# Optimization experiments

Hardware: AMD Instinct MI355X
Metric: run time of the kernel (lower is better)

## Reference

```python
import jax, jax.numpy as jnp
import numpy as np

N, E, G = 30000, 120000, 256
F_IN, F_E, H, T = 16, 8, 32, 10
EPS = 1e-5


def setup_inputs() -> dict:
    key = jax.random.key(0)
    ks = jax.random.split(key, 16)
    s = 0.05
    inp = {
        'x': jax.random.normal(ks[0], (N, F_IN), jnp.float32),
        'edge_attr': jax.random.normal(ks[1], (E, F_E), jnp.float32),
        'edge_index': jax.random.randint(ks[2], (2, E), 0, N),
        'batch': jnp.sort(jax.random.randint(ks[3], (N,), 0, G)),
        'c1_nn_w': jax.random.normal(ks[4], (F_E, F_IN * H), jnp.float32) * s,
        'c1_nn_b': jnp.zeros((F_IN * H,), jnp.float32),
        'c1_root': jax.random.normal(ks[5], (F_IN, H), jnp.float32) * s,
        'c1_bias': jnp.zeros((H,), jnp.float32),
        'c2_nn_w': jax.random.normal(ks[6], (F_E, H * H), jnp.float32) * s,
        'c2_nn_b': jnp.zeros((H * H,), jnp.float32),
        'c2_root': jax.random.normal(ks[7], (H, H), jnp.float32) * s,
        'c2_bias': jnp.zeros((H,), jnp.float32),
        'c3_nn_w': jax.random.normal(ks[8], (F_E, H * H), jnp.float32) * s,
        'c3_nn_b': jnp.zeros((H * H,), jnp.float32),
        'c3_root': jax.random.normal(ks[9], (H, H), jnp.float32) * s,
        'c3_bias': jnp.zeros((H,), jnp.float32),
        'bn1_g': jnp.ones((H,), jnp.float32), 'bn1_b': jnp.zeros((H,), jnp.float32),
        'bn1_m': jnp.zeros((H,), jnp.float32), 'bn1_v': jnp.ones((H,), jnp.float32),
        'bn2_g': jnp.ones((H,), jnp.float32), 'bn2_b': jnp.zeros((H,), jnp.float32),
        'bn2_m': jnp.zeros((H,), jnp.float32), 'bn2_v': jnp.ones((H,), jnp.float32),
        'mlp_w1': jax.random.normal(ks[10], (H, H), jnp.float32) * s,
        'mlp_b1': jnp.zeros((H,), jnp.float32),
        'mlp_w2': jax.random.normal(ks[11], (H, T), jnp.float32) * s,
        'mlp_b2': jnp.zeros((T,), jnp.float32),
    }
    return inp


def _nnconv(x, edge_index, edge_attr, nn_w, nn_b, root, bias, in_dim, out_dim):
    # per-edge weight matrix from edge features: [E, in_dim, out_dim]
    W = (edge_attr @ nn_w + nn_b).reshape(-1, in_dim, out_dim)
    # gather source node features, per-edge matvec, scatter-add to targets
    msg = jnp.einsum('ei,eio->eo', x[edge_index[0]], W)
    agg = jax.ops.segment_sum(msg, edge_index[1], num_segments=N)
    return agg + x @ root + bias


def _graph_size_norm(x, batch):
    deg = jax.ops.segment_sum(jnp.ones((N,), x.dtype), batch, num_segments=G)
    inv_sqrt = jnp.where(deg > 0, deg, 1.0) ** -0.5
    return x * inv_sqrt[batch][:, None]


def _bn_eval(x, g, b, m, v):
    return (x - m) * (g * jax.lax.rsqrt(v + EPS)) + b


def reference(x, edge_attr, edge_index, batch,
              c1_nn_w, c1_nn_b, c1_root, c1_bias,
              c2_nn_w, c2_nn_b, c2_root, c2_bias,
              c3_nn_w, c3_nn_b, c3_root, c3_bias,
              bn1_g, bn1_b, bn1_m, bn1_v,
              bn2_g, bn2_b, bn2_m, bn2_v,
              mlp_w1, mlp_b1, mlp_w2, mlp_b2):
    h = _nnconv(x, edge_index, edge_attr, c1_nn_w, c1_nn_b, c1_root, c1_bias, F_IN, H)
    h = _graph_size_norm(h, batch)
    h = jax.nn.relu(_bn_eval(h, bn1_g, bn1_b, bn1_m, bn1_v))
    h = _nnconv(h, edge_index, edge_attr, c2_nn_w, c2_nn_b, c2_root, c2_bias, H, H)
    h = _graph_size_norm(h, batch)
    h = jax.nn.relu(_bn_eval(h, bn2_g, bn2_b, bn2_m, bn2_v))
    h = _nnconv(h, edge_index, edge_attr, c3_nn_w, c3_nn_b, c3_root, c3_bias, H, H)
    # global mean pool over graphs
    cnt = jax.ops.segment_sum(jnp.ones((N,), h.dtype), batch, num_segments=G)
    pooled = jax.ops.segment_sum(h, batch, num_segments=G) / jnp.maximum(cnt, 1.0)[:, None]
    # MLP head (dropout inactive in eval)
    out = jax.nn.relu(pooled @ mlp_w1 + mlp_b1) @ mlp_w2 + mlp_b2
    return out
```

## Files before the change

### kernel.cpp

```cpp
#include <hip/hip_runtime.h>

#define NN 30000
#define NE 120000
#define NG 256
#define FIN 16
#define HD 32
#define TOUT 10
#define EPSV 1e-5f
#define NB_SCAN 30

__device__ __forceinline__ void atomAddF(float* p, float v) {
    unsafeAtomicAdd(p, v);
}

__global__ __launch_bounds__(256) void count_deg_kernel(
    const int* __restrict__ eidx, const int* __restrict__ batch,
    int* __restrict__ deg_in, float* __restrict__ deg_g)
{
    const int t = blockIdx.x * 256 + threadIdx.x;
    if (t < NE) atomicAdd(&deg_in[eidx[NE + t]], 1);

    const int lane = threadIdx.x & 63;
    const int g = (t < NN) ? batch[t] : -1;
    const int prev = __shfl_up(g, 1);
    const bool head = (lane == 0) || (g != prev);
    const unsigned long long heads = __ballot(head);
    if (head && g >= 0) {
        const unsigned long long higher =
            (lane < 63) ? (heads >> (lane + 1)) : 0ULL;
        const int next = higher ? (lane + __ffsll(higher)) : 64;
        atomAddF(&deg_g[g], (float)(next - lane));
    }
}

__global__ __launch_bounds__(1024) void scan_phase1(
    const int* __restrict__ deg_in, int* __restrict__ row_start,
    int* __restrict__ blocksum)
{
    __shared__ int wsum[16];
    const int t = threadIdx.x, lane = t & 63, w = t >> 6;
    const int idx = blockIdx.x * 1024 + t;
    const int v = (idx < NN) ? deg_in[idx] : 0;
    int s = v;
    #pragma unroll
    for (int off = 1; off < 64; off <<= 1) {
        const int u = __shfl_up(s, off, 64);
        if (lane >= off) s += u;
    }
    if (lane == 63) wsum[w] = s;
    __syncthreads();
    if (w == 0) {
        int ws = (lane < 16) ? wsum[lane] : 0;
        #pragma unroll
        for (int off = 1; off < 16; off <<= 1) {
            const int u = __shfl_up(ws, off, 64);
            if (lane >= off) ws += u;
        }
        if (lane < 16) wsum[lane] = ws;
    }
    __syncthreads();
    const int incl = s + ((w > 0) ? wsum[w - 1] : 0);
    if (idx < NN) row_start[idx] = incl - v;
    if (t == 1023) blocksum[blockIdx.x] = incl;
}

__global__ __launch_bounds__(1024) void scan_apply(
    const int* __restrict__ blocksum, int* __restrict__ row_start,
    int* __restrict__ cursor)
{
    __shared__ int boff_s;
    const int t = threadIdx.x;
    if (t < 64) {
        int v = (t < blockIdx.x) ? blocksum[t] : 0;
        #pragma unroll
        for (int off = 32; off > 0; off >>= 1) v += __shfl_down(v, off, 64);
        if (t == 0) boff_s = v;
    }
    __syncthreads();
    const int idx = blockIdx.x * 1024 + t;
    if (idx < NN) {
        const int r = row_start[idx] + boff_s;
        row_start[idx] = r;
        cursor[idx]    = r;
    }
    if (blockIdx.x == 0 && t == 0) row_start[NN] = NE;
}

__global__ __launch_bounds__(256) void csr_scatter(
    const int* __restrict__ eidx, const float* __restrict__ ea,
    int* __restrict__ cursor,
    int* __restrict__ src_s,
    float4* __restrict__ ea_s)
{
    const int e = blockIdx.x * 256 + threadIdx.x;
    if (e < NE) {
        const int d = eidx[NE + e];
        const int slot = atomicAdd(&cursor[d], 1);
        src_s[slot] = eidx[e];
        const float4* s4 = (const float4*)(ea + (size_t)e * 8);
        ea_s[2 * slot]     = s4[0];
        ea_s[2 * slot + 1] = s4[1];
    }
    if (e < 8) src_s[NE + e] = 0;
}

template<int IN, bool FINAL>
__global__ __launch_bounds__(256, 8) void fused_layer(
    const float* __restrict__ hin,
    const int*   __restrict__ src_s,
    const float4* __restrict__ ea_s,
    const int*   __restrict__ row_start,
    const float* __restrict__ nn_w,
    const float* __restrict__ nn_b,
    const float* __restrict__ root,
    const float* __restrict__ bias,
    const int*   __restrict__ batch,
    const float* __restrict__ deg_g,
    const float* __restrict__ bn_g,
    const float* __restrict__ bn_b,
    const float* __restrict__ bn_m,
    const float* __restrict__ bn_v,
    float*       __restrict__ out)
{
    constexpr int K  = 10 * IN;
    constexpr int KQ = K / 4;
    constexpr int KL = KQ / 2;
    constexpr int NQ = 32 / IN;

    __shared__ float Tlds[16 * K];
    __shared__ float Acc[16 * 32];

    const int tid = threadIdx.x;
    const int wv  = tid >> 6;
    const int l   = tid & 63;
    const int h   = l >> 5;
    const int o   = l & 31;
    const int l5  = l & 31;
    const int pr  = l >> 5;

    Acc[tid]       = bias[tid & 31];
    Acc[256 + tid] = bias[tid & 31];

    const int i = l5 & (IN - 1);
    const int q = l5 / IN;

    #pragma unroll
    for (int j = 0; j < 2; ++j) {
        const int nloc = wv * 4 + j * 2 + pr;
        const int d    = blockIdx.x * 16 + nloc;

        float t[9];
        #pragma unroll
        for (int f = 0; f < 9; ++f) t[f] = 0.0f;

        const int p0 = row_start[d];
        const int p1 = row_start[d + 1];

        int p = p0 + q;
        if (p < p1) {
            int pn     = p + NQ;
            int s_cur  = src_s[p];
            int s_nxt  = src_s[pn];
            float4 a_c = ea_s[2 * p];
            float4 b_c = ea_s[2 * p + 1];
            float  xv  = hin[(long)s_cur * IN + i];

            while (true) {
                const float4 a_n = ea_s[2 * pn];
                const float4 b_n = ea_s[2 * pn + 1];
                const float  xvn = hin[(long)s_nxt * IN + i];
                const int pn2    = pn + NQ;
                const int s_n2   = src_s[pn2];

                t[0] = fmaf(a_c.x, xv, t[0]);
                t[1] = fmaf(a_c.y, xv, t[1]);
                t[2] = fmaf(a_c.z, xv, t[2]);
                t[3] = fmaf(a_c.w, xv, t[3]);
                t[4] = fmaf(b_c.x, xv, t[4]);
                t[5] = fmaf(b_c.y, xv, t[5]);
                t[6] = fmaf(b_c.z, xv, t[6]);
                t[7] = fmaf(b_c.w, xv, t[7]);
                t[8] += xv;

                p = pn;
                if (p >= p1) break;
                pn = pn2; s_nxt = s_n2;
                a_c = a_n; b_c = b_n; xv = xvn;
            }
        }

        if (IN == 16) {
            #pragma unroll
            for (int f = 0; f < 9; ++f) t[f] += __shfl_xor(t[f], 16, 64);
        }

        if (l5 < IN) {
            float* tb = Tlds + nloc * K;
            #pragma unroll
            for (int f = 0; f < 9; ++f) tb[f * IN + i] = t[f];
            tb[9 * IN + i] = hin[(long)d * IN + i];
        }
    }
    __syncthreads();

    float Wreg[KL];
    const int kbase = wv * KQ + h * KL;
    #pragma unroll
    for (int kk = 0; kk < KL; ++kk) {
        const int k = kbase + kk;
        const float* src = (k < 8 * IN) ? (nn_w + k * 32)
                         : (k < 9 * IN) ? (nn_b + (k - 8 * IN) * 32)
                                        : (root + (k - 9 * IN) * 32);
        Wreg[kk] = src[o];
    }

    for (int n = 0; n < 16; ++n) {
        const float* tb = Tlds + n * K + kbase;
        float acc = 0.0f;
        #pragma unroll
        for (int kq = 0; kq < KL / 4; ++kq) {
            const float4 tv = *(const float4*)(tb + kq * 4);
            acc = fmaf(Wreg[4 * kq + 0], tv.x, acc);
            acc = fmaf(Wreg[4 * kq + 1], tv.y, acc);
            acc = fmaf(Wreg[4 * kq + 2], tv.z, acc);
            acc = fmaf(Wreg[4 * kq + 3], tv.w, acc);
        }
        acc += __shfl_xor(acc, 32, 64);
        if (h == 0) atomicAdd(&Acc[n * 32 + o], acc);
    }
    __syncthreads();

    #pragma unroll
    for (int r = 0; r < 2; ++r) {
        const int idx = r * 256 + tid;
        const int n   = idx >> 5;
        const int oo  = idx & 31;
        float sum = Acc[idx];
        const int d = blockIdx.x * 16 + n;
        const int g = batch[d];
        if (!FINAL) {
            float dg = deg_g[g];
            dg = dg > 0.0f ? dg : 1.0f;
            float v = sum * (1.0f / sqrtf(dg));
            const float s = bn_g[oo] / sqrtf(bn_v[oo] + EPSV);
            v = (v - bn_m[oo]) * s + bn_b[oo];
            out[(long)d * 32 + oo] = v > 0.0f ? v : 0.0f;
        } else {
            float v = sum;
            const int   g2 = __shfl(g, (tid & 63) ^ 32, 64);
            const float v2 = __shfl(v, (tid & 63) ^ 32, 64);
            bool do_store = true;
            if (g2 == g) {
                if (tid & 32) do_store = false;
                else          v += v2;
            }
            if (do_store) atomAddF(&out[g * 32 + oo], v);
        }
    }
}

__global__ __launch_bounds__(64) void head_kernel(
    const float* __restrict__ pooled,
    const float* __restrict__ deg,
    const float* __restrict__ w1,
    const float* __restrict__ b1,
    const float* __restrict__ w2,
    const float* __restrict__ b2,
    float*       __restrict__ out)
{
    const int g = blockIdx.x * 64 + threadIdx.x;
    if (g >= NG) return;
    float cnt = deg[g];
    cnt = cnt > 1.0f ? cnt : 1.0f;

    float p[HD];
    #pragma unroll
    for (int i = 0; i < HD; ++i) p[i] = pooled[g * HD + i] / cnt;

    float hid[HD];
    #pragma unroll
    for (int j = 0; j < HD; ++j) {
        float a = b1[j];
        #pragma unroll
        for (int i = 0; i < HD; ++i)
            a = fmaf(p[i], w1[i * HD + j], a);
        hid[j] = a > 0.0f ? a : 0.0f;
    }
    #pragma unroll
    for (int t = 0; t < TOUT; ++t) {
        float a = b2[t];
        #pragma unroll
        for (int j = 0; j < HD; ++j)
            a = fmaf(hid[j], w2[j * TOUT + t], a);
        out[g * TOUT + t] = a;
    }
}

extern "C" void kernel_launch(void* const* d_in, const int* in_sizes, int n_in,
                              void* d_out, int out_size, void* d_ws, size_t ws_size,
                              hipStream_t stream)
{
    const float* x        = (const float*)d_in[0];
    const float* ea       = (const float*)d_in[1];
    const int*   eidx     = (const int*)  d_in[2];
    const int*   batch    = (const int*)  d_in[3];
    const float* c1_nn_w  = (const float*)d_in[4];
    const float* c1_nn_b  = (const float*)d_in[5];
    const float* c1_root  = (const float*)d_in[6];
    const float* c1_bias  = (const float*)d_in[7];
    const float* c2_nn_w  = (const float*)d_in[8];
    const float* c2_nn_b  = (const float*)d_in[9];
    const float* c2_root  = (const float*)d_in[10];
    const float* c2_bias  = (const float*)d_in[11];
    const float* c3_nn_w  = (const float*)d_in[12];
    const float* c3_nn_b  = (const float*)d_in[13];
    const float* c3_root  = (const float*)d_in[14];
    const float* c3_bias  = (const float*)d_in[15];
    const float* bn1_g    = (const float*)d_in[16];
    const float* bn1_b    = (const float*)d_in[17];
    const float* bn1_m    = (const float*)d_in[18];
    const float* bn1_v    = (const float*)d_in[19];
    const float* bn2_g    = (const float*)d_in[20];
    const float* bn2_b    = (const float*)d_in[21];
    const float* bn2_m    = (const float*)d_in[22];
    const float* bn2_v    = (const float*)d_in[23];
    const float* mlp_w1   = (const float*)d_in[24];
    const float* mlp_b1   = (const float*)d_in[25];
    const float* mlp_w2   = (const float*)d_in[26];
    const float* mlp_b2   = (const float*)d_in[27];
    float* out = (float*)d_out;

    float4* ea_s   = (float4*)d_ws;
    int*    src_s  = (int*)(ea_s + 2 * (NE + 8));
    float*  h1     = (float*)(src_s + NE + 8);
    float*  h2     = h1 + NN * HD;
    int*    deg_in = (int*)(h2 + NN * HD);
    float*  deg_g  = (float*)(deg_in + NN);
    float*  pooled = deg_g + NG;
    int*    row_s  = (int*)(pooled + NG * HD);
    int*    cursor = row_s + NN + 1;
    int*    bsum   = cursor + NN;

    hipMemsetAsync(deg_in, 0, sizeof(int) * (NN + NG + NG * HD), stream);

    const int egrid = (NE + 255) / 256;

    count_deg_kernel<<<egrid, 256, 0, stream>>>(eidx, batch, deg_in, deg_g);
    scan_phase1<<<NB_SCAN, 1024, 0, stream>>>(deg_in, row_s, bsum);
    scan_apply <<<NB_SCAN, 1024, 0, stream>>>(bsum, row_s, cursor);
    csr_scatter<<<egrid, 256, 0, stream>>>(eidx, ea, cursor, src_s, ea_s);

    const int lgrid = NN / 16;

    fused_layer<FIN, false><<<lgrid, 256, 0, stream>>>(
        x, src_s, ea_s, row_s, c1_nn_w, c1_nn_b, c1_root, c1_bias,
        batch, deg_g, bn1_g, bn1_b, bn1_m, bn1_v, h1);

    fused_layer<HD, false><<<lgrid, 256, 0, stream>>>(
        h1, src_s, ea_s, row_s, c2_nn_w, c2_nn_b, c2_root, c2_bias,
        batch, deg_g, bn2_g, bn2_b, bn2_m, bn2_v, h2);

    fused_layer<HD, true><<<lgrid, 256, 0, stream>>>(
        h2, src_s, ea_s, row_s, c3_nn_w, c3_nn_b, c3_root, c3_bias,
        batch, deg_g, nullptr, nullptr, nullptr, nullptr, pooled);

    head_kernel<<<(NG + 63) / 64, 64, 0, stream>>>(pooled, deg_g, mlp_w1, mlp_b1,
                                                   mlp_w2, mlp_b2, out);
}
```

Measured before the change: 274.6 us.

## Distribute block's edges flat across threads with LDS atomic accumulation

Instead of assigning a fixed group of lanes to each destination node, each block now walks the contiguous range of all edges belonging to its 16 nodes, with threads striding by 256/IN edges. Partial products go straight into padded shared-memory rows through LDS atomics, and the CSR now stores (src,dst) pairs so each edge knows its target row. The aim is to remove load imbalance and idle lanes on nodes with few or many edges. The cost is nine shared atomics per edge per feature, possible contention when edges hit the same row, and a larger edge array.

```diff
diff --git a/kernel.cpp b/kernel.cpp
--- a/kernel.cpp
+++ b/kernel.cpp
@@ -89,25 +89,30 @@
 __global__ __launch_bounds__(256) void csr_scatter(
     const int* __restrict__ eidx, const float* __restrict__ ea,
     int* __restrict__ cursor,
-    int* __restrict__ src_s,
+    int2* __restrict__ sd_s,
     float4* __restrict__ ea_s)
 {
     const int e = blockIdx.x * 256 + threadIdx.x;
     if (e < NE) {
+        const int s = eidx[e];
         const int d = eidx[NE + e];
         const int slot = atomicAdd(&cursor[d], 1);
-        src_s[slot] = eidx[e];
+        sd_s[slot] = make_int2(s, d);
         const float4* s4 = (const float4*)(ea + (size_t)e * 8);
         ea_s[2 * slot]     = s4[0];
         ea_s[2 * slot + 1] = s4[1];
     }
-    if (e < 8) src_s[NE + e] = 0;
+    if (e < 32) {
+        sd_s[NE + e] = make_int2(0, 0);
+        ea_s[2 * (NE + e)]     = make_float4(0.f, 0.f, 0.f, 0.f);
+        ea_s[2 * (NE + e) + 1] = make_float4(0.f, 0.f, 0.f, 0.f);
+    }
 }
 
 template<int IN, bool FINAL>
 __global__ __launch_bounds__(256, 8) void fused_layer(
     const float* __restrict__ hin,
-    const int*   __restrict__ src_s,
+    const int2*  __restrict__ sd_s,
     const float4* __restrict__ ea_s,
     const int*   __restrict__ row_start,
     const float* __restrict__ nn_w,
@@ -122,83 +127,77 @@
     const float* __restrict__ bn_v,
     float*       __restrict__ out)
 {
-    constexpr int K  = 10 * IN;
-    constexpr int KQ = K / 4;
-    constexpr int KL = KQ / 2;
-    constexpr int NQ = 32 / IN;
-
-    __shared__ float Tlds[16 * K];
+    constexpr int K   = 10 * IN;
+    constexpr int KP  = K + 4;
+    constexpr int KQ  = K / 4;
+    constexpr int KL  = K / 8;
+    constexpr int EPG = 256 / IN;
+
+    __shared__ float Tlds[16 * KP];
     __shared__ float Acc[16 * 32];
 
-    const int tid = threadIdx.x;
-    const int wv  = tid >> 6;
-    const int l   = tid & 63;
-    const int h   = l >> 5;
-    const int o   = l & 31;
-    const int l5  = l & 31;
-    const int pr  = l >> 5;
-
-    Acc[tid]       = bias[tid & 31];
-    Acc[256 + tid] = bias[tid & 31];
-
-    const int i = l5 & (IN - 1);
-    const int q = l5 / IN;
-
-    #pragma unroll
-    for (int j = 0; j < 2; ++j) {
-        const int nloc = wv * 4 + j * 2 + pr;
-        const int d    = blockIdx.x * 16 + nloc;
-
-        float t[9];
-        #pragma unroll
-        for (int f = 0; f < 9; ++f) t[f] = 0.0f;
-
-        const int p0 = row_start[d];
-        const int p1 = row_start[d + 1];
-
-        int p = p0 + q;
-        if (p < p1) {
-            int pn     = p + NQ;
-            int s_cur  = src_s[p];
-            int s_nxt  = src_s[pn];
-            float4 a_c = ea_s[2 * p];
-            float4 b_c = ea_s[2 * p + 1];
-            float  xv  = hin[(long)s_cur * IN + i];
+    const int tid  = threadIdx.x;
+    const int wv   = tid >> 6;
+    const int l    = tid & 63;
+    const int h    = l >> 5;
+    const int o    = l & 31;
+    const int base = blockIdx.x * 16;
+
+    {
+        float4* tz = (float4*)Tlds;
+        constexpr int NZ4 = (16 * 9 * IN) / 4;
+        constexpr int C4  = (9 * IN) / 4;
+        for (int idx = tid; idx < NZ4; idx += 256) {
+            const int n = idx / C4;
+            const int c = idx % C4;
+            tz[n * (KP / 4) + c] = make_float4(0.f, 0.f, 0.f, 0.f);
+        }
+        #pragma unroll
+        for (int r = 0; r < (16 * IN) / 256; ++r) {
+            const int idx = r * 256 + tid;
+            Tlds[(idx / IN) * KP + 9 * IN + (idx % IN)] =
+                hin[(long)base * IN + idx];
+        }
+        Acc[tid]       = bias[o];
+        Acc[256 + tid] = bias[o];
+    }
+    __syncthreads();
+
+    {
+        const int i = tid % IN;
+        const int s = tid / IN;
+        const int e0 = row_start[base];
+        const int e1 = row_start[base + 16];
+
+        int p = e0 + s;
+        if (p < e1) {
+            int2   sd_c = sd_s[p];
+            float4 a_c  = ea_s[2 * p];
+            float4 b_c  = ea_s[2 * p + 1];
+            float  xv   = hin[(long)sd_c.x * IN + i];
 
             while (true) {
-                const float4 a_n = ea_s[2 * pn];
-                const float4 b_n = ea_s[2 * pn + 1];
-                const float  xvn = hin[(long)s_nxt * IN + i];
-                const int pn2    = pn + NQ;
-                const int s_n2   = src_s[pn2];
-
-                t[0] = fmaf(a_c.x, xv, t[0]);
-                t[1] = fmaf(a_c.y, xv, t[1]);
-                t[2] = fmaf(a_c.z, xv, t[2]);
-                t[3] = fmaf(a_c.w, xv, t[3]);
-                t[4] = fmaf(b_c.x, xv, t[4]);
-                t[5] = fmaf(b_c.y, xv, t[5]);
-                t[6] = fmaf(b_c.z, xv, t[6]);
-                t[7] = fmaf(b_c.w, xv, t[7]);
-                t[8] += xv;
+                const int pn = p + EPG;
+                const int2   sd_n = sd_s[pn];
+                const float4 a_n  = ea_s[2 * pn];
+                const float4 b_n  = ea_s[2 * pn + 1];
+                const float  xvn  = hin[(long)sd_n.x * IN + i];
+
+                float* tr = Tlds + (sd_c.y - base) * KP + i;
+                atomicAdd(tr + 0 * IN, a_c.x * xv);
+                atomicAdd(tr + 1 * IN, a_c.y * xv);
+                atomicAdd(tr + 2 * IN, a_c.z * xv);
+                atomicAdd(tr + 3 * IN, a_c.w * xv);
+                atomicAdd(tr + 4 * IN, b_c.x * xv);
+                atomicAdd(tr + 5 * IN, b_c.y * xv);
+                atomicAdd(tr + 6 * IN, b_c.z * xv);
+                atomicAdd(tr + 7 * IN, b_c.w * xv);
+                atomicAdd(tr + 8 * IN, xv);
 
                 p = pn;
-                if (p >= p1) break;
-                pn = pn2; s_nxt = s_n2;
-                a_c = a_n; b_c = b_n; xv = xvn;
+                if (p >= e1) break;
+                sd_c = sd_n; a_c = a_n; b_c = b_n; xv = xvn;
             }
-        }
-
-        if (IN == 16) {
-            #pragma unroll
-            for (int f = 0; f < 9; ++f) t[f] += __shfl_xor(t[f], 16, 64);
-        }
-
-        if (l5 < IN) {
-            float* tb = Tlds + nloc * K;
-            #pragma unroll
-            for (int f = 0; f < 9; ++f) tb[f * IN + i] = t[f];
-            tb[9 * IN + i] = hin[(long)d * IN + i];
         }
     }
     __syncthreads();
@@ -215,7 +214,7 @@
     }
 
     for (int n = 0; n < 16; ++n) {
-        const float* tb = Tlds + n * K + kbase;
+        const float* tb = Tlds + n * KP + kbase;
         float acc = 0.0f;
         #pragma unroll
         for (int kq = 0; kq < KL / 4; ++kq) {
@@ -236,7 +235,7 @@
         const int n   = idx >> 5;
         const int oo  = idx & 31;
         float sum = Acc[idx];
-        const int d = blockIdx.x * 16 + n;
+        const int d = base + n;
         const int g = batch[d];
         if (!FINAL) {
             float dg = deg_g[g];
@@ -330,9 +329,9 @@
     const float* mlp_b2   = (const float*)d_in[27];
     float* out = (float*)d_out;
 
-    float4* ea_s   = (float4*)d_ws;
-    int*    src_s  = (int*)(ea_s + 2 * (NE + 8));
-    float*  h1     = (float*)(src_s + NE + 8);
+    int2*   sd_s   = (int2*)d_ws;
+    float4* ea_s   = (float4*)(sd_s + NE + 32);
+    float*  h1     = (float*)(ea_s + 2 * (NE + 32));
     float*  h2     = h1 + NN * HD;
     int*    deg_in = (int*)(h2 + NN * HD);
     float*  deg_g  = (float*)(deg_in + NN);
@@ -348,20 +347,20 @@
     count_deg_kernel<<<egrid, 256, 0, stream>>>(eidx, batch, deg_in, deg_g);
     scan_phase1<<<NB_SCAN, 1024, 0, stream>>>(deg_in, row_s, bsum);
     scan_apply <<<NB_SCAN, 1024, 0, stream>>>(bsum, row_s, cursor);
-    csr_scatter<<<egrid, 256, 0, stream>>>(eidx, ea, cursor, src_s, ea_s);
+    csr_scatter<<<egrid, 256, 0, stream>>>(eidx, ea, cursor, sd_s, ea_s);
 
     const int lgrid = NN / 16;
 
     fused_layer<FIN, false><<<lgrid, 256, 0, stream>>>(
-        x, src_s, ea_s, row_s, c1_nn_w, c1_nn_b, c1_root, c1_bias,
+        x, sd_s, ea_s, row_s, c1_nn_w, c1_nn_b, c1_root, c1_bias,
         batch, deg_g, bn1_g, bn1_b, bn1_m, bn1_v, h1);
 
     fused_layer<HD, false><<<lgrid, 256, 0, stream>>>(
-        h1, src_s, ea_s, row_s, c2_nn_w, c2_nn_b, c2_root, c2_bias,
+        h1, sd_s, ea_s, row_s, c2_nn_w, c2_nn_b, c2_root, c2_bias,
         batch, deg_g, bn2_g, bn2_b, bn2_m, bn2_v, h2);
 
     fused_layer<HD, true><<<lgrid, 256, 0, stream>>>(
-        h2, src_s, ea_s, row_s, c3_nn_w, c3_nn_b, c3_root, c3_bias,
+        h2, sd_s, ea_s, row_s, c3_nn_w, c3_nn_b, c3_root, c3_bias,
         batch, deg_g, nullptr, nullptr, nullptr, nullptr, pooled);
 
     head_kernel<<<(NG + 63) / 64, 64, 0, stream>>>(pooled, deg_g, mlp_w1, mlp_b1,
```

Result: slower. 755.7 us (+175.2%).
